# Optimization experiments

Hardware: AMD Instinct MI355X
Metric: run time of the kernel (lower is better)

The kernel has to match this reference:

```python
import jax, jax.numpy as jnp
import numpy as np

R, N, B, S = 20, 4096, 16, 256          # relations, total nodes, graphs, nodes per graph
DIN, HID, H = 512, 128, 4               # in_dim, hidden_dim, num_heads
D = HID * H                              # flattened node-feature width (=512)
E = 16384                                # edges per relation
NEG_SLOPE = 0.2


def _gat(h, src, dst, W, al, ar, b):
    # DGL GATConv, eval mode (dropout off), identity residual (in == H*out), allow_zero_in_degree
    z = (h @ W).reshape(N, H, HID)                        # [N,H,Dh]
    el = (z * al).sum(-1)                                 # [N,H]
    er = (z * ar).sum(-1)                                 # [N,H]
    e = jax.nn.leaky_relu(el[src] + er[dst], NEG_SLOPE)   # [E,H]
    m = jax.ops.segment_max(e, dst, num_segments=N)       # per-dst max (edge softmax)
    ex = jnp.exp(e - m[dst])
    den = jax.ops.segment_sum(ex, dst, num_segments=N)
    alpha = ex / den[dst]                                 # [E,H]
    agg = jax.ops.segment_sum(alpha[..., None] * z[src], dst, num_segments=N)
    return agg + h.reshape(N, H, HID) + b, alpha


def _rgat_conv(h, src, dst, W, al, ar, b):
    # HeteroGraphConv with aggregate='mean' over R relations; scan keeps memory flat
    def body(acc, xs):
        s, d, Wr, alr, arr, br = xs
        out, alpha = _gat(h, s, d, Wr, alr, arr, br)
        return acc + out, alpha.mean(-1)                  # attention meaned over heads -> [E]
    acc, attn = jax.lax.scan(body, jnp.zeros((N, H, HID), h.dtype), (src, dst, W, al, ar, b))
    return acc / R, attn                                  # [N,H,Dh], [R,E]


def setup_inputs() -> dict:
    key = jax.random.key(0)
    ks = jax.random.split(key, 24)
    f32 = jnp.float32
    p = lambda k, shape: jax.random.normal(k, shape, f32) * 0.05
    z = lambda shape: jnp.zeros(shape, f32)
    return {
        'feat': jax.random.normal(ks[0], (N, DIN), f32),
        'hyp_emb': jax.random.normal(ks[1], (B, D), f32),
        'edge_src': jax.random.randint(ks[2], (R, E), 0, N),
        'edge_dst': jax.random.randint(ks[3], (R, E), 0, N),
        'W1': p(ks[4], (R, DIN, H * HID)), 'al1': p(ks[5], (R, H, HID)), 'ar1': p(ks[6], (R, H, HID)), 'b1': z((R, H, HID)),
        'W2': p(ks[7], (R, D, H * HID)), 'al2': p(ks[8], (R, H, HID)), 'ar2': p(ks[9], (R, H, HID)), 'b2': z((R, H, HID)),
        'Wq': p(ks[10], (D, D)), 'bq': z(D), 'Wk': p(ks[11], (D, D)), 'bk': z(D),
        'Wv': p(ks[12], (D, D)), 'bv': z(D), 'Wo': p(ks[13], (D, D)), 'bo': z(D),
        'Wn1': p(ks[14], (2 * D, HID)), 'bn1': z(HID), 'Wn2': p(ks[15], (HID, 2)), 'bn2': z(2),
    }


def reference(feat, hyp_emb, edge_src, edge_dst,
              W1, al1, ar1, b1, W2, al2, ar2, b2,
              Wq, bq, Wk, bk, Wv, bv, Wo, bo, Wn1, bn1, Wn2, bn2):
    # --- RGAT (rgat_generation) layer 1 + attention weights ---
    h1, attn = _rgat_conv(feat, edge_src, edge_dst, W1, al1, ar1, b1)
    h1 = jax.nn.elu(h1.reshape(N, D))
    # --- layer 2 ---
    h2, _ = _rgat_conv(h1, edge_src, edge_dst, W2, al2, ar2, b2)
    feats = h2.reshape(N, D)
    # --- node importance: scatter-add edge attention onto dst nodes, summed over etypes ---
    imp = jax.ops.segment_sum(attn.reshape(-1), edge_dst.reshape(-1), num_segments=N)
    feats_p = feats.reshape(B, S, D)                      # uniform graphs: split+pad == reshape
    weighted = feats_p * imp.reshape(B, S)[..., None]
    # --- MultiheadAttention(embed=D, heads=4): query = hyp_emb broadcast to all S positions ---
    Hm, Dm = 4, D // 4
    q = (hyp_emb @ Wq + bq).reshape(B, Hm, 1, Dm)         # identical query at every position
    k = (feats_p @ Wk + bk).reshape(B, S, Hm, Dm).transpose(0, 2, 1, 3)
    v = (feats_p @ Wv + bv).reshape(B, S, Hm, Dm).transpose(0, 2, 1, 3)
    scores = jnp.einsum('bhqd,bhkd->bhqk', q, k) / jnp.sqrt(jnp.float32(Dm))
    a = jax.nn.softmax(scores, axis=-1)                   # [B,Hm,1,S]
    ctx = jnp.einsum('bhqk,bhkd->bhqd', a, v).reshape(B, 1, D)
    attn_out = jnp.broadcast_to(ctx @ Wo + bo, (B, S, D))
    # --- node classifier on concat(weighted feats, attention output) ---
    combined = jnp.concatenate([weighted, attn_out], axis=-1).reshape(N, 2 * D)
    node_logits = jax.nn.relu(combined @ Wn1 + bn1) @ Wn2 + bn2
    return node_logits, attn
```

## Files before the change

### kernel.cpp

```cpp
#include <hip/hip_runtime.h>
#include <hip/hip_bf16.h>
#include <math.h>

#define NREL 20
#define NN   4096
#define NE   16384
#define DF   512
#define NHD  4
#define DHH  128
#define NB   16
#define NS   256

typedef __attribute__((ext_vector_type(8))) __bf16 bf16x8;
typedef __attribute__((ext_vector_type(4))) float f32x4;
typedef __attribute__((ext_vector_type(2))) float f32x2;

struct f8 { unsigned char b; };

__device__ inline float bf2f(unsigned short u) {
    union { float f; unsigned int i; } c; c.i = ((unsigned int)u) << 16; return c.f;
}
__device__ inline unsigned short f2bu(float f) {
    union { __hip_bfloat16 b; unsigned short u; } c; c.b = __float2bfloat16(f); return c.u;
}
__device__ inline void storeOut(float* p, float v) { *p = v; }
__device__ inline void storeOut(__hip_bfloat16* p, float v) { *p = __float2bfloat16(v); }

__device__ inline void load_lds16(const __hip_bfloat16* g, __hip_bfloat16* l) {
    __builtin_amdgcn_global_load_lds(
        (const __attribute__((address_space(1))) unsigned int*)(const void*)g,
        (__attribute__((address_space(3))) unsigned int*)(void*)l, 16, 0, 0);
}

__device__ inline int kswz(int f, int row) { return f ^ (((row) & 7) << 3); }

__global__ __launch_bounds__(256) void prep_kernel(
    const float* __restrict__ feat, unsigned short* __restrict__ featbf,
    const float* __restrict__ b1, const float* __restrict__ b2,
    const float* __restrict__ bk, const float* __restrict__ bv,
    float* __restrict__ bsum1, float* __restrict__ bsum2,
    float* __restrict__ bkv, int* __restrict__ cnt, float* __restrict__ imp)
{
    int blk = blockIdx.x, t = threadIdx.x;
    if (blk < 1024) {
        int idx = blk * 256 + t;
        int row = idx >> 6;
        int f = (idx & 63) * 8;
        int fs = kswz(f, row);
        const float4* ip = (const float4*)&feat[(size_t)row * DF + f];
        float4 v0 = ip[0], v1 = ip[1];
        union { unsigned short u[8]; uint4 q; } o;
        o.u[0] = f2bu(v0.x); o.u[1] = f2bu(v0.y); o.u[2] = f2bu(v0.z); o.u[3] = f2bu(v0.w);
        o.u[4] = f2bu(v1.x); o.u[5] = f2bu(v1.y); o.u[6] = f2bu(v1.z); o.u[7] = f2bu(v1.w);
        *(uint4*)(featbf + (size_t)row * DF + fs) = o.q;
    } else if (blk == 1024) {
        #pragma unroll
        for (int rep = 0; rep < 2; ++rep) {
            int f = t + rep * 256;
            float s1 = 0.f, s2 = 0.f;
            #pragma unroll
            for (int r = 0; r < NREL; ++r) { s1 += b1[r * DF + f]; s2 += b2[r * DF + f]; }
            bsum1[f] = s1; bsum2[f] = s2;
        }
        for (int i = t; i < NN; i += 256) imp[i] = 0.f;
    } else if (blk == 1025) {
        #pragma unroll
        for (int j = 0; j < 4; ++j) {
            int f = t + j * 256;
            bkv[f] = (f < DF) ? bk[f] : bv[f - DF];
        }
    } else {
        int idx = (blk - 1026) * 256 + t;
        cnt[idx] = 0;
    }
}

__global__ void count_kernel(const int* __restrict__ dst, int* __restrict__ cnt) {
    int idx = blockIdx.x * 256 + threadIdx.x;
    int r = idx / NE;
    atomicAdd(&cnt[r * NN + dst[idx]], 1);
}

__global__ void scan_kernel(const int* __restrict__ cnt, int* __restrict__ rowptr,
                            int* __restrict__ woff, int* __restrict__ rowptr2,
                            int* __restrict__ croff) {
    int r = blockIdx.x;
    int t = threadIdx.x;
    __shared__ int sums[1024];
    int v[4]; int local = 0;
    if (r < NREL) {
        #pragma unroll
        for (int j = 0; j < 4; ++j) { v[j] = cnt[r * NN + t * 4 + j]; local += v[j]; }
    } else {
        #pragma unroll
        for (int j = 0; j < 4; ++j) {
            int s = 0;
            for (int rel = 0; rel < NREL; ++rel) {
                croff[rel * NN + t * 4 + j] = s;
                s += cnt[rel * NN + t * 4 + j];
            }
            v[j] = s; local += s;
        }
    }
    sums[t] = local;
    __syncthreads();
    for (int off = 1; off < 1024; off <<= 1) {
        int x = (t >= off) ? sums[t - off] : 0;
        __syncthreads();
        sums[t] += x;
        __syncthreads();
    }
    int run = (t == 0) ? 0 : sums[t - 1];
    if (r < NREL) {
        #pragma unroll
        for (int j = 0; j < 4; ++j) {
            rowptr[r * (NN + 1) + t * 4 + j] = run;
            woff[r * NN + t * 4 + j] = run;
            run += v[j];
        }
        if (t == 1023) rowptr[r * (NN + 1) + NN] = run;
    } else {
        #pragma unroll
        for (int j = 0; j < 4; ++j) { rowptr2[t * 4 + j] = run; run += v[j]; }
        if (t == 1023) rowptr2[NN] = run;
    }
}

__global__ void fill_kernel(const int* __restrict__ dst, const int* __restrict__ src,
                            int* __restrict__ woff, int* __restrict__ srcCSR,
                            int* __restrict__ eidCSR) {
    int idx = blockIdx.x * 256 + threadIdx.x;
    int r = idx / NE; int e = idx % NE;
    int pos = atomicAdd(&woff[r * NN + dst[idx]], 1);
    srcCSR[r * NE + pos] = src[idx];
    eidCSR[r * NE + pos] = e;
}

__global__ __launch_bounds__(256) void transw_kernel(
    const float* __restrict__ W, __hip_bfloat16* __restrict__ Wt, int K, int N)
{
    int r = blockIdx.z;
    __shared__ float t[32][33];
    int k0 = blockIdx.x * 32, n0 = blockIdx.y * 32;
    int tx = threadIdx.x % 32, ty = threadIdx.x / 32;
    #pragma unroll
    for (int kk = ty; kk < 32; kk += 8)
        t[kk][tx] = W[((size_t)r * K + k0 + kk) * N + n0 + tx];
    __syncthreads();
    #pragma unroll
    for (int nn = ty; nn < 32; nn += 8) {
        int row = n0 + nn;
        Wt[((size_t)r * N + row) * K + kswz(k0 + tx, row)] = __float2bfloat16(t[tx][nn]);
    }
}

__global__ __launch_bounds__(256) void transw2_kernel(
    const float* __restrict__ W1, const float* __restrict__ W2,
    __hip_bfloat16* __restrict__ Wt1, __hip_bfloat16* __restrict__ Wt2)
{
    int z = blockIdx.z;
    const float* W = (z < NREL) ? W1 : W2;
    __hip_bfloat16* Wt = (z < NREL) ? Wt1 : Wt2;
    int r = (z < NREL) ? z : z - NREL;
    __shared__ float t[32][33];
    int k0 = blockIdx.x * 32, n0 = blockIdx.y * 32;
    int tx = threadIdx.x % 32, ty = threadIdx.x / 32;
    #pragma unroll
    for (int kk = ty; kk < 32; kk += 8)
        t[kk][tx] = W[((size_t)r * DF + k0 + kk) * DF + n0 + tx];
    __syncthreads();
    #pragma unroll
    for (int nn = ty; nn < 32; nn += 8) {
        int row = n0 + nn;
        Wt[((size_t)r * DF + row) * DF + kswz(k0 + tx, row)] = __float2bfloat16(t[tx][nn]);
    }
}

__global__ __launch_bounds__(256) void transw_kv_kernel(
    const float* __restrict__ Wk, const float* __restrict__ Wv,
    __hip_bfloat16* __restrict__ Wt)
{
    int z = blockIdx.z;
    const float* W = z ? Wv : Wk;
    __shared__ float t[32][33];
    int k0 = blockIdx.x * 32, n0 = blockIdx.y * 32;
    int tx = threadIdx.x % 32, ty = threadIdx.x / 32;
    #pragma unroll
    for (int kk = ty; kk < 32; kk += 8)
        t[kk][tx] = W[(size_t)(k0 + kk) * DF + n0 + tx];
    __syncthreads();
    #pragma unroll
    for (int nn = ty; nn < 32; nn += 8) {
        int row = n0 + nn;
        Wt[((size_t)z * DF + row) * DF + kswz(k0 + tx, row)] = __float2bfloat16(t[tx][nn]);
    }
}

template <typename OutT, bool RELU, bool FUSE, bool SPLITK = false>
__global__ __launch_bounds__(256) void mfma_gemm(
    const __hip_bfloat16* __restrict__ A,
    const __hip_bfloat16* __restrict__ BtAll,
    const float* __restrict__ bias, int biasStride,
    OutT* __restrict__ Call, int M, int N, int K, int lda,
    const float* __restrict__ al, const float* __restrict__ ar,
    float* __restrict__ el, float* __restrict__ er)
{
    int r = blockIdx.z;
    const __hip_bfloat16* Bt;
    int koff;
    if (SPLITK) { Bt = BtAll;                         koff = r * K; }
    else        { Bt = BtAll + (size_t)r * N * lda;   koff = 0; }
    OutT* C = Call + (size_t)r * M * N;
    const int rowBase = blockIdx.y * 128;
    const int colBase = blockIdx.x * 128;
    __shared__ __hip_bfloat16 As[128 * 64];
    __shared__ __hip_bfloat16 Bs[128 * 64];
    const int tid = threadIdx.x;
    const int w = tid >> 6, l = tid & 63;
    const int wr = w >> 1, wc = w & 1;
    const int m15 = l & 15, q = l >> 4;
    const int sRow = tid >> 3;
    const int sChk = tid & 7;
    const __hip_bfloat16* Ag = A + (size_t)(rowBase + sRow) * lda + koff + sChk * 8;
    const __hip_bfloat16* Bg = Bt + (size_t)(colBase + sRow) * lda + koff + sChk * 8;
    __hip_bfloat16* Asl = As + tid * 8;
    __hip_bfloat16* Bsl = Bs + tid * 8;
    const int swr = m15 & 7;

    f32x4 acc[4][4];
    #pragma unroll
    for (int i = 0; i < 4; ++i)
        #pragma unroll
        for (int j = 0; j < 4; ++j) acc[i][j] = (f32x4){0.f, 0.f, 0.f, 0.f};

    for (int k0 = 0; k0 < K; k0 += 64) {
        #pragma unroll
        for (int c = 0; c < 4; ++c) {
            load_lds16(Ag + (size_t)c * 32 * lda + k0, Asl + c * 2048);
            load_lds16(Bg + (size_t)c * 32 * lda + k0, Bsl + c * 2048);
        }
        __syncthreads();
        #pragma unroll
        for (int g = 0; g < 2; ++g) {
            bf16x8 a[4], b[4];
            #pragma unroll
            for (int i = 0; i < 4; ++i)
                a[i] = *(const bf16x8*)&As[(wr * 64 + i * 16 + m15) * 64 + ((g * 4 + q) ^ swr) * 8];
            #pragma unroll
            for (int j = 0; j < 4; ++j)
                b[j] = *(const bf16x8*)&Bs[(wc * 64 + j * 16 + m15) * 64 + ((g * 4 + q) ^ swr) * 8];
            #pragma unroll
            for (int i = 0; i < 4; ++i)
                #pragma unroll
                for (int j = 0; j < 4; ++j)
                    acc[i][j] = __builtin_amdgcn_mfma_f32_16x16x32_bf16(a[i], b[j], acc[i][j], 0, 0, 0);
        }
        __syncthreads();
    }

    if constexpr (sizeof(OutT) == 1) {
        unsigned char* cbuf = (unsigned char*)As;
        #pragma unroll
        for (int i = 0; i < 4; ++i)
            #pragma unroll
            for (int j = 0; j < 4; ++j) {
                int colL = wc * 64 + j * 16 + m15;
                #pragma unroll
                for (int reg = 0; reg < 4; ++reg) {
                    int rowL = wr * 64 + i * 16 + q * 4 + reg;
                    unsigned int pk = __builtin_amdgcn_cvt_pk_fp8_f32(
                        acc[i][j][reg], acc[i][j][reg], 0, false);
                    cbuf[rowL * 128 + colL] = (unsigned char)(pk & 0xFF);
                }
            }
        __syncthreads();
        int rowL = tid >> 1, colL = (tid & 1) * 64;
        const uint4* src = (const uint4*)&cbuf[rowL * 128 + colL];
        uint4* dst = (uint4*)((unsigned char*)C + (size_t)(rowBase + rowL) * N
                              + colBase + colL);
        #pragma unroll
        for (int x = 0; x < 4; ++x) dst[x] = src[x];
    } else {
        #pragma unroll
        for (int i = 0; i < 4; ++i) {
            #pragma unroll
            for (int j = 0; j < 4; ++j) {
                int col = colBase + wc * 64 + j * 16 + m15;
                float bv = bias ? bias[r * biasStride + col] : 0.f;
                #pragma unroll
                for (int reg = 0; reg < 4; ++reg) {
                    int row = rowBase + wr * 64 + i * 16 + q * 4 + reg;
                    float v = acc[i][j][reg] + bv;
                    if (RELU) v = fmaxf(v, 0.f);
                    storeOut(&C[(size_t)row * N + col], v);
                }
            }
        }
    }

    if (FUSE) {
        float alv[4], arv[4];
        #pragma unroll
        for (int j = 0; j < 4; ++j) {
            int col = colBase + wc * 64 + j * 16 + m15;
            alv[j] = al[r * DF + col];
            arv[j] = ar[r * DF + col];
        }
        float pe[4][4], pr[4][4];
        #pragma unroll
        for (int i = 0; i < 4; ++i)
            #pragma unroll
            for (int reg = 0; reg < 4; ++reg) {
                float se = 0.f, sr = 0.f;
                #pragma unroll
                for (int j = 0; j < 4; ++j) {
                    se += acc[i][j][reg] * alv[j];
                    sr += acc[i][j][reg] * arv[j];
                }
                pe[i][reg] = se; pr[i][reg] = sr;
            }
        #pragma unroll
        for (int off = 1; off < 16; off <<= 1)
            #pragma unroll
            for (int i = 0; i < 4; ++i)
                #pragma unroll
                for (int reg = 0; reg < 4; ++reg) {
                    pe[i][reg] += __shfl_xor(pe[i][reg], off);
                    pr[i][reg] += __shfl_xor(pr[i][reg], off);
                }
        float* eP = (float*)Bs;
        float* rP = eP + 256;
        if (m15 == 0) {
            #pragma unroll
            for (int i = 0; i < 4; ++i)
                #pragma unroll
                for (int reg = 0; reg < 4; ++reg) {
                    int rowL = wr * 64 + i * 16 + q * 4 + reg;
                    eP[rowL * 2 + wc] = pe[i][reg];
                    rP[rowL * 2 + wc] = pr[i][reg];
                }
        }
        __syncthreads();
        if (tid < 128) {
            int head = colBase >> 7;
            size_t idx = ((size_t)r * NN + rowBase + tid) * NHD + head;
            el[idx] = eP[tid * 2] + eP[tid * 2 + 1];
            er[idx] = rP[tid * 2] + rP[tid * 2 + 1];
        }
    }
}

template <typename OutT>
__global__ __launch_bounds__(256) void gemm_kernel(
    const float* __restrict__ A, const float* __restrict__ Bm,
    const float* __restrict__ bias, OutT* __restrict__ C,
    int M, int K, int Nn)
{
    int r = blockIdx.z;
    const float* B = Bm + (size_t)r * K * Nn;
    OutT* Cr = C + (size_t)r * M * Nn;
    int rowBase = blockIdx.y * 64;
    int colBase = blockIdx.x * 64;
    __shared__ float As[64][17];
    __shared__ float Bs[16][64];
    int tid = threadIdx.x;
    int tx = tid % 16, ty = tid / 16;
    float acc[4][4] = {};
    int aRow = tid / 4, aK4 = (tid % 4) * 4;
    int bK = tid / 16, bN4 = (tid % 16) * 4;
    for (int k0 = 0; k0 < K; k0 += 16) {
        int gRow = rowBase + aRow;
        float4 av = make_float4(0.f, 0.f, 0.f, 0.f);
        if (gRow < M) av = *(const float4*)(A + (size_t)gRow * K + k0 + aK4);
        As[aRow][aK4 + 0] = av.x; As[aRow][aK4 + 1] = av.y;
        As[aRow][aK4 + 2] = av.z; As[aRow][aK4 + 3] = av.w;
        float4 bv = *(const float4*)(B + (size_t)(k0 + bK) * Nn + colBase + bN4);
        *(float4*)&Bs[bK][bN4] = bv;
        __syncthreads();
        #pragma unroll
        for (int k = 0; k < 16; ++k) {
            float a[4], b[4];
            #pragma unroll
            for (int i = 0; i < 4; ++i) a[i] = As[ty * 4 + i][k];
            #pragma unroll
            for (int j = 0; j < 4; ++j) b[j] = Bs[k][tx * 4 + j];
            #pragma unroll
            for (int i = 0; i < 4; ++i)
                #pragma unroll
                for (int j = 0; j < 4; ++j) acc[i][j] += a[i] * b[j];
        }
        __syncthreads();
    }
    #pragma unroll
    for (int i = 0; i < 4; ++i) {
        int gRow = rowBase + ty * 4 + i;
        if (gRow >= M) continue;
        #pragma unroll
        for (int j = 0; j < 4; ++j) {
            int gCol = colBase + tx * 4 + j;
            float v = acc[i][j];
            if (bias) v += bias[gCol];
            storeOut(&Cr[(size_t)gRow * Nn + gCol], v);
        }
    }
}

__global__ __launch_bounds__(256) void alpha_kernel(
    const float* __restrict__ el, const float* __restrict__ er,
    const int* __restrict__ rowptr, const int* __restrict__ rowptr2,
    const int* __restrict__ croff, const int* __restrict__ srcCSR,
    const int* __restrict__ eidCSR,
    float* __restrict__ alphaPk, int* __restrict__ srcPk,
    float* __restrict__ attn, float* __restrict__ imp)
{
    int t = blockIdx.x * 256 + threadIdx.x;
    int r = t / NN, n = t % NN;
    int start = rowptr[r * (NN + 1) + n];
    int d = rowptr[r * (NN + 1) + n + 1] - start;
    if (d == 0) return;
    int pbase = rowptr2[n] + croff[r * NN + n];
    float4 er4 = *(const float4*)&er[((size_t)r * NN + n) * NHD];
    float4 den = make_float4(0.f, 0.f, 0.f, 0.f);
    for (int j = 0; j < d; ++j) {
        int s = srcCSR[r * NE + start + j];
        float4 el4 = *(const float4*)&el[((size_t)r * NN + s) * NHD];
        float v0 = el4.x + er4.x; v0 = v0 > 0.f ? v0 : 0.2f * v0;
        float v1 = el4.y + er4.y; v1 = v1 > 0.f ? v1 : 0.2f * v1;
        float v2 = el4.z + er4.z; v2 = v2 > 0.f ? v2 : 0.2f * v2;
        float v3 = el4.w + er4.w; v3 = v3 > 0.f ? v3 : 0.2f * v3;
        float4 e4 = make_float4(__expf(v0), __expf(v1), __expf(v2), __expf(v3));
        den.x += e4.x; den.y += e4.y; den.z += e4.z; den.w += e4.w;
        *(float4*)&alphaPk[(size_t)(pbase + j) * 4] = e4;
        srcPk[pbase + j] = r * NN + s;
    }
    float4 inv = make_float4(1.f / den.x, 1.f / den.y, 1.f / den.z, 1.f / den.w);
    float impLoc = 0.f;
    for (int j = 0; j < d; ++j) {
        float4 a4 = *(const float4*)&alphaPk[(size_t)(pbase + j) * 4];
        a4.x *= inv.x; a4.y *= inv.y; a4.z *= inv.z; a4.w *= inv.w;
        *(float4*)&alphaPk[(size_t)(pbase + j) * 4] = a4;
        if (attn) {
            float a = 0.25f * (a4.x + a4.y + a4.z + a4.w);
            attn[r * NE + eidCSR[r * NE + start + j]] = a;
            impLoc += a;
        }
    }
    if (attn) atomicAdd(&imp[n], impLoc);
}

__global__ __launch_bounds__(256) void aggc_kernel(
    const unsigned char* __restrict__ Z,
    const int* __restrict__ rowptr2, const int* __restrict__ srcPk,
    const float* __restrict__ alphaPk, const float* __restrict__ bsum,
    const float* __restrict__ hin, float* __restrict__ hout,
    __hip_bfloat16* __restrict__ hout_bf, int applyElu)
{
    int n = blockIdx.x;
    int w = threadIdx.x >> 6, lane = threadIdx.x & 63;
    int h = lane >> 4;
    int base = rowptr2[n];
    int deg = rowptr2[n + 1] - base;
    float acc[8] = {};
    if (deg > 0) {
        int i = w * 4;
        int zz[4]; float aa[4];
        #pragma unroll
        for (int j = 0; j < 4; ++j) {
            int idx = i + j; int cidx = idx < deg ? idx : deg - 1;
            zz[j] = srcPk[base + cidx];
            aa[j] = (idx < deg) ? alphaPk[(size_t)(base + cidx) * 4 + h] : 0.f;
        }
        while (i < deg) {
            int cz[4]; float ca[4];
            #pragma unroll
            for (int j = 0; j < 4; ++j) { cz[j] = zz[j]; ca[j] = aa[j]; }
            int ni = i + 16;
            #pragma unroll
            for (int j = 0; j < 4; ++j) {
                int idx = ni + j; int cidx = idx < deg ? idx : deg - 1;
                zz[j] = srcPk[base + cidx];
                aa[j] = (idx < deg) ? alphaPk[(size_t)(base + cidx) * 4 + h] : 0.f;
            }
            uint2 raw[4];
            #pragma unroll
            for (int j = 0; j < 4; ++j)
                raw[j] = *(const uint2*)&Z[(size_t)cz[j] * DF + lane * 8];
            #pragma unroll
            for (int j = 0; j < 4; ++j) {
                f32x2 f01 = __builtin_amdgcn_cvt_pk_f32_fp8((int)raw[j].x, false);
                f32x2 f23 = __builtin_amdgcn_cvt_pk_f32_fp8((int)raw[j].x, true);
                f32x2 f45 = __builtin_amdgcn_cvt_pk_f32_fp8((int)raw[j].y, false);
                f32x2 f67 = __builtin_amdgcn_cvt_pk_f32_fp8((int)raw[j].y, true);
                acc[0] += ca[j] * f01.x; acc[1] += ca[j] * f01.y;
                acc[2] += ca[j] * f23.x; acc[3] += ca[j] * f23.y;
                acc[4] += ca[j] * f45.x; acc[5] += ca[j] * f45.y;
                acc[6] += ca[j] * f67.x; acc[7] += ca[j] * f67.y;
            }
            i = ni;
        }
    }
    __shared__ float red[4][DF];
    #pragma unroll
    for (int j = 0; j < 8; ++j) red[w][lane * 8 + j] = acc[j];
    __syncthreads();
    const float invR = 1.0f / NREL;
    const int sw = (n & 7) << 3;
    int f = threadIdx.x;
    #pragma unroll
    for (int rep = 0; rep < 2; ++rep, f += 256) {
        float v = red[0][f] + red[1][f] + red[2][f] + red[3][f];
        v = (v + bsum[f]) * invR + hin[(size_t)n * DF + f];
        if (applyElu) v = v > 0.f ? v : expm1f(v);
        hout[(size_t)n * DF + f] = v;
        hout_bf[(size_t)n * DF + (f ^ sw)] = __float2bfloat16(v);
    }
}

__global__ __launch_bounds__(256) void mha_scores(
    const float* __restrict__ q, const float* __restrict__ k,
    float* __restrict__ scores)
{
    int b = blockIdx.x;
    int w = threadIdx.x >> 6, lane = threadIdx.x & 63;
    int s = blockIdx.y * 4 + w;
    const float4* qp = (const float4*)&q[(size_t)b * DF + lane * 8];
    const float4* kp = (const float4*)&k[((size_t)(b * NS + s)) * DF + lane * 8];
    float4 q0 = qp[0], q1 = qp[1];
    float4 k0 = kp[0], k1 = kp[1];
    float p = q0.x * k0.x + q0.y * k0.y + q0.z * k0.z + q0.w * k0.w
            + q1.x * k1.x + q1.y * k1.y + q1.z * k1.z + q1.w * k1.w;
    #pragma unroll
    for (int off = 1; off < 16; off <<= 1) p += __shfl_xor(p, off);
    if ((lane & 15) == 0) {
        int h = lane >> 4;
        scores[((size_t)(b * NHD + h)) * NS + s] = p * 0.08838834764831845f;
    }
}

__global__ __launch_bounds__(256) void mha_soft(float* __restrict__ scores) {
    int b = blockIdx.x;
    int h = threadIdx.x >> 6, lane = threadIdx.x & 63;
    float* sp = &scores[((size_t)(b * NHD + h)) * NS];
    float v[4];
    float mx = -INFINITY;
    #pragma unroll
    for (int i = 0; i < 4; ++i) { v[i] = sp[lane + 64 * i]; mx = fmaxf(mx, v[i]); }
    #pragma unroll
    for (int off = 32; off; off >>= 1) mx = fmaxf(mx, __shfl_xor(mx, off));
    float sum = 0.f;
    #pragma unroll
    for (int i = 0; i < 4; ++i) { v[i] = __expf(v[i] - mx); sum += v[i]; }
    #pragma unroll
    for (int off = 32; off; off >>= 1) sum += __shfl_xor(sum, off);
    float inv = 1.0f / sum;
    #pragma unroll
    for (int i = 0; i < 4; ++i) sp[lane + 64 * i] = v[i] * inv;
}

__global__ __launch_bounds__(256) void mha_ctx(
    const float* __restrict__ scores, const float* __restrict__ v,
    float* __restrict__ ctx)
{
    int b = blockIdx.x, h = blockIdx.y;
    int t = threadIdx.x;
    int d = t & 127, half = t >> 7;
    __shared__ float a_s[NS];
    a_s[t] = scores[((size_t)(b * NHD + h)) * NS + t];
    __syncthreads();
    float acc = 0.f;
    const float* vp = &v[((size_t)(b * NS + half * 128)) * DF + h * DHH + d];
    #pragma unroll 4
    for (int i = 0; i < 128; ++i)
        acc += a_s[half * 128 + i] * vp[(size_t)i * DF];
    __shared__ float red[256];
    red[t] = acc;
    __syncthreads();
    if (t < 128) ctx[(size_t)b * DF + h * DHH + t] = red[t] + red[t + 128];
}

__global__ __launch_bounds__(256) void combined_kernel(
    const float* __restrict__ feats, const float* __restrict__ imp,
    const float* __restrict__ abuf, __hip_bfloat16* __restrict__ comb)
{
    int n = blockIdx.x;
    int t = threadIdx.x;
    int b = n >> 8;
    float im = imp[n];
    const int sw = (n & 7) << 3;
    #pragma unroll
    for (int rep = 0; rep < 4; ++rep) {
        int f = t + rep * 256;
        float v = (f < DF) ? feats[(size_t)n * DF + f] * im
                           : abuf[(size_t)b * DF + (f - DF)];
        comb[(size_t)n * (2 * DF) + (f ^ sw)] = __float2bfloat16(v);
    }
}

__global__ __launch_bounds__(256) void cls2_kernel(
    const float* __restrict__ hidden4, const float* __restrict__ bn1,
    const float* __restrict__ Wn2, const float* __restrict__ bn2,
    float* __restrict__ out)
{
    __shared__ float w2[256];
    __shared__ float b1s[128];
    int t = threadIdx.x;
    w2[t] = Wn2[t];
    if (t < 128) b1s[t] = bn1[t];
    __syncthreads();
    int n = blockIdx.x * 256 + t;
    const float* hp = &hidden4[(size_t)n * 128];
    const size_t ps = (size_t)NN * 128;
    float p0 = bn2[0], p1 = bn2[1];
    #pragma unroll 4
    for (int kk = 0; kk < 128; ++kk) {
        float hv = hp[kk] + hp[ps + kk] + hp[2 * ps + kk] + hp[3 * ps + kk] + b1s[kk];
        hv = fmaxf(hv, 0.f);
        p0 += hv * w2[kk * 2 + 0];
        p1 += hv * w2[kk * 2 + 1];
    }
    out[n * 2 + 0] = p0;
    out[n * 2 + 1] = p1;
}

extern "C" void kernel_launch(void* const* d_in, const int* in_sizes, int n_in,
                              void* d_out, int out_size, void* d_ws, size_t ws_size,
                              hipStream_t stream) {
    const float* feat = (const float*)d_in[0];
    const float* hyp  = (const float*)d_in[1];
    const int*   esrc = (const int*)d_in[2];
    const int*   edst = (const int*)d_in[3];
    const float* W1   = (const float*)d_in[4];
    const float* al1  = (const float*)d_in[5];
    const float* ar1  = (const float*)d_in[6];
    const float* b1   = (const float*)d_in[7];
    const float* W2   = (const float*)d_in[8];
    const float* al2  = (const float*)d_in[9];
    const float* ar2  = (const float*)d_in[10];
    const float* b2   = (const float*)d_in[11];
    const float* Wq = (const float*)d_in[12]; const float* bq = (const float*)d_in[13];
    const float* Wk = (const float*)d_in[14]; const float* bk = (const float*)d_in[15];
    const float* Wv = (const float*)d_in[16]; const float* bv = (const float*)d_in[17];
    const float* Wo = (const float*)d_in[18]; const float* bo = (const float*)d_in[19];
    const float* Wn1 = (const float*)d_in[20]; const float* bn1 = (const float*)d_in[21];
    const float* Wn2 = (const float*)d_in[22]; const float* bn2 = (const float*)d_in[23];

    char* ws = (char*)d_ws;
    size_t off = 0;
    auto alloc = [&](size_t bytes) -> void* {
        void* p = ws + off;
        off += (bytes + 255) & ~(size_t)255;
        return p;
    };
    unsigned char* Z = (unsigned char*)alloc((size_t)NREL * NN * DF);
    float* el     = (float*)alloc((size_t)NREL * NN * NHD * 4);
    float* er     = (float*)alloc((size_t)NREL * NN * NHD * 4);
    int* rowptr   = (int*)alloc((size_t)NREL * (NN + 1) * 4);
    int* rowptr2  = (int*)alloc((size_t)(NN + 1) * 4);
    int* woff     = (int*)alloc((size_t)NREL * NN * 4);
    int* srcCSR   = (int*)alloc((size_t)NREL * NE * 4);
    int* eidCSR   = (int*)alloc((size_t)NREL * NE * 4);
    int* cnt      = (int*)alloc((size_t)NREL * NN * 4);
    int* croff    = (int*)alloc((size_t)NREL * NN * 4);
    int* srcPk    = (int*)alloc((size_t)NREL * NE * 4);
    float* alphaPk= (float*)alloc((size_t)NREL * NE * NHD * 4);
    float* bsum1  = (float*)alloc((size_t)DF * 4);
    float* bsum2  = (float*)alloc((size_t)DF * 4);
    float* bkv    = (float*)alloc((size_t)2 * DF * 4);
    float* h1     = (float*)alloc((size_t)NN * DF * 4);
    float* feats  = (float*)alloc((size_t)NN * DF * 4);
    float* imp    = (float*)alloc((size_t)NN * 4);
    float* kvbuf  = (float*)alloc((size_t)2 * NN * DF * 4);
    float* qbuf   = (float*)alloc((size_t)NB * DF * 4);
    float* ctxb   = (float*)alloc((size_t)NB * DF * 4);
    float* abuf   = (float*)alloc((size_t)NB * DF * 4);
    float* scoresb= (float*)alloc((size_t)NB * NHD * NS * 4);
    float* hidden4= (float*)alloc((size_t)4 * NN * 128 * 4);
    __hip_bfloat16* featbf  = (__hip_bfloat16*)alloc((size_t)NN * DF * 2);
    __hip_bfloat16* h1bf    = (__hip_bfloat16*)alloc((size_t)NN * DF * 2);
    __hip_bfloat16* featsbf = (__hip_bfloat16*)alloc((size_t)NN * DF * 2);
    __hip_bfloat16* combbf  = (__hip_bfloat16*)alloc((size_t)NN * 2 * DF * 2);
    __hip_bfloat16* Wt1 = (__hip_bfloat16*)alloc((size_t)NREL * DF * DF * 2);
    __hip_bfloat16* Wt2 = (__hip_bfloat16*)alloc((size_t)NREL * DF * DF * 2);
    __hip_bfloat16* WtKV = (__hip_bfloat16*)alloc((size_t)2 * DF * DF * 2);
    __hip_bfloat16* Wn1t = (__hip_bfloat16*)alloc((size_t)(2 * DF) * 128 * 2);
    if (off > ws_size) return;

    float* logits = (float*)d_out;
    float* attn   = (float*)d_out + (size_t)NN * 2;
    float* kbuf = kvbuf;
    float* vbuf = kvbuf + (size_t)NN * DF;

    prep_kernel<<<1026 + NREL * NN / 256, 256, 0, stream>>>(
        feat, (unsigned short*)featbf, b1, b2, bk, bv, bsum1, bsum2, bkv, cnt, imp);

    count_kernel<<<NREL * NE / 256, 256, 0, stream>>>(edst, cnt);
    scan_kernel<<<NREL + 1, 1024, 0, stream>>>(cnt, rowptr, woff, rowptr2, croff);
    fill_kernel<<<NREL * NE / 256, 256, 0, stream>>>(edst, esrc, woff, srcCSR, eidCSR);

    transw2_kernel<<<dim3(DF / 32, DF / 32, 2 * NREL), 256, 0, stream>>>(W1, W2, Wt1, Wt2);
    transw_kv_kernel<<<dim3(DF / 32, DF / 32, 2), 256, 0, stream>>>(Wk, Wv, WtKV);
    transw_kernel<<<dim3(2 * DF / 32, 128 / 32, 1), 256, 0, stream>>>(Wn1, Wn1t, 2 * DF, 128);

    mfma_gemm<f8, false, true><<<dim3(DF / 128, NN / 128, NREL), 256, 0, stream>>>(
        featbf, Wt1, nullptr, 0, (f8*)Z, NN, DF, DF, DF, al1, ar1, el, er);
    alpha_kernel<<<NREL * NN / 256, 256, 0, stream>>>(
        el, er, rowptr, rowptr2, croff, srcCSR, eidCSR, alphaPk, srcPk, attn, imp);
    aggc_kernel<<<NN, 256, 0, stream>>>(Z, rowptr2, srcPk, alphaPk, bsum1,
                                        feat, h1, h1bf, 1);

    mfma_gemm<f8, false, true><<<dim3(DF / 128, NN / 128, NREL), 256, 0, stream>>>(
        h1bf, Wt2, nullptr, 0, (f8*)Z, NN, DF, DF, DF, al2, ar2, el, er);
    alpha_kernel<<<NREL * NN / 256, 256, 0, stream>>>(
        el, er, rowptr, rowptr2, croff, srcCSR, eidCSR, alphaPk, srcPk, nullptr, nullptr);
    aggc_kernel<<<NN, 256, 0, stream>>>(Z, rowptr2, srcPk, alphaPk, bsum2,
                                        h1, feats, featsbf, 0);

    mfma_gemm<float, false, false><<<dim3(DF / 128, NN / 128, 2), 256, 0, stream>>>(
        featsbf, WtKV, bkv, DF, kvbuf, NN, DF, DF, DF, nullptr, nullptr, nullptr, nullptr);
    gemm_kernel<float><<<dim3(DF / 64, 1, 1), 256, 0, stream>>>(
        hyp, Wq, bq, qbuf, NB, DF, DF);
    mha_scores<<<dim3(NB, NS / 4), 256, 0, stream>>>(qbuf, kbuf, scoresb);
    mha_soft<<<NB, 256, 0, stream>>>(scoresb);
    mha_ctx<<<dim3(NB, NHD), 256, 0, stream>>>(scoresb, vbuf, ctxb);
    gemm_kernel<float><<<dim3(DF / 64, 1, 1), 256, 0, stream>>>(
        ctxb, Wo, bo, abuf, NB, DF, DF);

    combined_kernel<<<NN, 256, 0, stream>>>(feats, imp, abuf, combbf);
    mfma_gemm<float, false, false, true><<<dim3(1, NN / 128, 4), 256, 0, stream>>>(
        combbf, Wn1t, nullptr, 0, hidden4, NN, 128, 256, 2 * DF,
        nullptr, nullptr, nullptr, nullptr);
    cls2_kernel<<<NN / 256, 256, 0, stream>>>(hidden4, bn1, Wn2, bn2, logits);
}
```

Measured before the change: 577.4 us.

## Replace per-relation GAT projection GEMM with 256x256 double-buffered MFMA kernel

Adds a specialized zgemm8 kernel with 256x256 tiles, 512 threads, double-buffered LDS staging and interleaved MFMA phases. It emits FP8 Z through an LDS-staged coalesced store and fuses the el/er attention-logit reductions into the epilogue. The change also merges the K/V weight transpose into the W1/W2 transpose launch and folds the MHA softmax into mha_ctx, removing two launches. The larger tile improves operand reuse, but it cuts the grid to 2x16x20 blocks and raises register and LDS pressure, which may hurt occupancy.

```diff
diff --git a/kernel.cpp b/kernel.cpp
--- a/kernel.cpp
+++ b/kernel.cpp
@@ -156,43 +156,219 @@
 
 __global__ __launch_bounds__(256) void transw2_kernel(
     const float* __restrict__ W1, const float* __restrict__ W2,
-    __hip_bfloat16* __restrict__ Wt1, __hip_bfloat16* __restrict__ Wt2)
+    const float* __restrict__ Wk, const float* __restrict__ Wv,
+    __hip_bfloat16* __restrict__ Wt1, __hip_bfloat16* __restrict__ Wt2,
+    __hip_bfloat16* __restrict__ WtKV)
 {
     int z = blockIdx.z;
-    const float* W = (z < NREL) ? W1 : W2;
-    __hip_bfloat16* Wt = (z < NREL) ? Wt1 : Wt2;
-    int r = (z < NREL) ? z : z - NREL;
+    const float* Wsrc; __hip_bfloat16* Wdst;
+    if (z < NREL)           { Wsrc = W1 + (size_t)z * DF * DF;          Wdst = Wt1 + (size_t)z * DF * DF; }
+    else if (z < 2 * NREL)  { Wsrc = W2 + (size_t)(z - NREL) * DF * DF; Wdst = Wt2 + (size_t)(z - NREL) * DF * DF; }
+    else if (z == 2 * NREL) { Wsrc = Wk;                                Wdst = WtKV; }
+    else                    { Wsrc = Wv;                                Wdst = WtKV + (size_t)DF * DF; }
     __shared__ float t[32][33];
     int k0 = blockIdx.x * 32, n0 = blockIdx.y * 32;
     int tx = threadIdx.x % 32, ty = threadIdx.x / 32;
     #pragma unroll
     for (int kk = ty; kk < 32; kk += 8)
-        t[kk][tx] = W[((size_t)r * DF + k0 + kk) * DF + n0 + tx];
+        t[kk][tx] = Wsrc[(size_t)(k0 + kk) * DF + n0 + tx];
     __syncthreads();
     #pragma unroll
     for (int nn = ty; nn < 32; nn += 8) {
         int row = n0 + nn;
-        Wt[((size_t)r * DF + row) * DF + kswz(k0 + tx, row)] = __float2bfloat16(t[tx][nn]);
-    }
-}
-
-__global__ __launch_bounds__(256) void transw_kv_kernel(
-    const float* __restrict__ Wk, const float* __restrict__ Wv,
-    __hip_bfloat16* __restrict__ Wt)
-{
-    int z = blockIdx.z;
-    const float* W = z ? Wv : Wk;
-    __shared__ float t[32][33];
-    int k0 = blockIdx.x * 32, n0 = blockIdx.y * 32;
-    int tx = threadIdx.x % 32, ty = threadIdx.x / 32;
-    #pragma unroll
-    for (int kk = ty; kk < 32; kk += 8)
-        t[kk][tx] = W[(size_t)(k0 + kk) * DF + n0 + tx];
-    __syncthreads();
-    #pragma unroll
-    for (int nn = ty; nn < 32; nn += 8) {
-        int row = n0 + nn;
-        Wt[((size_t)z * DF + row) * DF + kswz(k0 + tx, row)] = __float2bfloat16(t[tx][nn]);
+        Wdst[(size_t)row * DF + kswz(k0 + tx, row)] = __float2bfloat16(t[tx][nn]);
+    }
+}
+
+__global__ __launch_bounds__(512) void zgemm8(
+    const __hip_bfloat16* __restrict__ A,
+    const __hip_bfloat16* __restrict__ BtAll,
+    unsigned char* __restrict__ Zall,
+    const float* __restrict__ al, const float* __restrict__ ar,
+    float* __restrict__ el, float* __restrict__ er)
+{
+    const int r = blockIdx.z;
+    const __hip_bfloat16* Bt = BtAll + (size_t)r * DF * DF;
+    unsigned char* Z = Zall + (size_t)r * NN * DF;
+    const int rowBase = blockIdx.y * 256;
+    const int colBase = blockIdx.x * 256;
+    __shared__ __hip_bfloat16 As[2][256][64];
+    __shared__ __hip_bfloat16 Bs[2][256][64];
+    const int tid = threadIdx.x;
+    const int w = tid >> 6, l = tid & 63;
+    const int wr = w >> 2, wc = w & 3;
+    const int m15 = l & 15, q = l >> 4;
+    const int swr = m15 & 7;
+
+    const __hip_bfloat16* Ag = A + (size_t)(rowBase + (tid >> 3)) * DF + (tid & 7) * 8;
+    const __hip_bfloat16* Bg = Bt + (size_t)(colBase + (tid >> 3)) * DF + (tid & 7) * 8;
+    __hip_bfloat16* AsT = &As[0][0][0] + tid * 8;
+    __hip_bfloat16* BsT = &Bs[0][0][0] + tid * 8;
+
+#define STAGE_A(buf, half, kt) do { \
+        const __hip_bfloat16* s_ = Ag + (size_t)((half) * 128) * DF + (kt) * 64; \
+        __hip_bfloat16* d_ = AsT + (buf) * 16384 + (half) * 8192; \
+        load_lds16(s_, d_); \
+        load_lds16(s_ + (size_t)64 * DF, d_ + 4096); } while (0)
+#define STAGE_B(buf, half, kt) do { \
+        const __hip_bfloat16* s_ = Bg + (size_t)((half) * 128) * DF + (kt) * 64; \
+        __hip_bfloat16* d_ = BsT + (buf) * 16384 + (half) * 8192; \
+        load_lds16(s_, d_); \
+        load_lds16(s_ + (size_t)64 * DF, d_ + 4096); } while (0)
+
+    f32x4 acc[8][4];
+    #pragma unroll
+    for (int i = 0; i < 8; ++i)
+        #pragma unroll
+        for (int j = 0; j < 4; ++j) acc[i][j] = (f32x4){0.f, 0.f, 0.f, 0.f};
+
+    const int NT = DF / 64;
+    STAGE_A(0, 0, 0); STAGE_A(0, 1, 0); STAGE_B(0, 0, 0); STAGE_B(0, 1, 0);
+    STAGE_A(1, 0, 1); STAGE_A(1, 1, 1);
+    asm volatile("s_waitcnt vmcnt(4)" ::: "memory");
+    __builtin_amdgcn_s_barrier();
+    __builtin_amdgcn_sched_barrier(0);
+
+    bf16x8 a0[8], a1[8], b0[4], b1[4];
+    for (int kt = 0; kt < NT; ++kt) {
+        const int buf = kt & 1, obuf = buf ^ 1;
+        #pragma unroll
+        for (int i = 0; i < 8; ++i)
+            a0[i] = *(const bf16x8*)&As[buf][wr * 128 + i * 16 + m15][(q ^ swr) * 8];
+        #pragma unroll
+        for (int j = 0; j < 4; ++j)
+            b0[j] = *(const bf16x8*)&Bs[buf][wc * 64 + j * 16 + m15][(q ^ swr) * 8];
+        if (kt + 1 < NT) STAGE_B(obuf, 0, kt + 1);
+        __builtin_amdgcn_s_barrier();
+        asm volatile("s_waitcnt lgkmcnt(0)" ::: "memory");
+        __builtin_amdgcn_sched_barrier(0);
+        __builtin_amdgcn_s_setprio(1);
+        #pragma unroll
+        for (int i = 0; i < 4; ++i)
+            #pragma unroll
+            for (int j = 0; j < 4; ++j)
+                acc[i][j] = __builtin_amdgcn_mfma_f32_16x16x32_bf16(a0[i], b0[j], acc[i][j], 0, 0, 0);
+        __builtin_amdgcn_s_setprio(0);
+        __builtin_amdgcn_s_barrier();
+        #pragma unroll
+        for (int i = 0; i < 8; ++i)
+            a1[i] = *(const bf16x8*)&As[buf][wr * 128 + i * 16 + m15][((4 + q) ^ swr) * 8];
+        if (kt + 1 < NT) STAGE_B(obuf, 1, kt + 1);
+        __builtin_amdgcn_s_barrier();
+        asm volatile("s_waitcnt lgkmcnt(0)" ::: "memory");
+        __builtin_amdgcn_sched_barrier(0);
+        __builtin_amdgcn_s_setprio(1);
+        #pragma unroll
+        for (int i = 4; i < 8; ++i)
+            #pragma unroll
+            for (int j = 0; j < 4; ++j)
+                acc[i][j] = __builtin_amdgcn_mfma_f32_16x16x32_bf16(a0[i], b0[j], acc[i][j], 0, 0, 0);
+        __builtin_amdgcn_s_setprio(0);
+        __builtin_amdgcn_s_barrier();
+        #pragma unroll
+        for (int j = 0; j < 4; ++j)
+            b1[j] = *(const bf16x8*)&Bs[buf][wc * 64 + j * 16 + m15][((4 + q) ^ swr) * 8];
+        if (kt + 2 < NT) STAGE_A(buf, 0, kt + 2);
+        __builtin_amdgcn_s_barrier();
+        asm volatile("s_waitcnt lgkmcnt(0)" ::: "memory");
+        __builtin_amdgcn_sched_barrier(0);
+        __builtin_amdgcn_s_setprio(1);
+        #pragma unroll
+        for (int i = 0; i < 4; ++i)
+            #pragma unroll
+            for (int j = 0; j < 4; ++j)
+                acc[i][j] = __builtin_amdgcn_mfma_f32_16x16x32_bf16(a1[i], b1[j], acc[i][j], 0, 0, 0);
+        __builtin_amdgcn_s_setprio(0);
+        __builtin_amdgcn_s_barrier();
+        if (kt + 2 < NT) STAGE_A(buf, 1, kt + 2);
+        __builtin_amdgcn_s_barrier();
+        __builtin_amdgcn_s_setprio(1);
+        #pragma unroll
+        for (int i = 4; i < 8; ++i)
+            #pragma unroll
+            for (int j = 0; j < 4; ++j)
+                acc[i][j] = __builtin_amdgcn_mfma_f32_16x16x32_bf16(a1[i], b1[j], acc[i][j], 0, 0, 0);
+        __builtin_amdgcn_s_setprio(0);
+        if (kt + 2 < NT) { asm volatile("s_waitcnt vmcnt(4)" ::: "memory"); }
+        else             { asm volatile("s_waitcnt vmcnt(0)" ::: "memory"); }
+        __builtin_amdgcn_s_barrier();
+        __builtin_amdgcn_sched_barrier(0);
+    }
+#undef STAGE_A
+#undef STAGE_B
+
+    unsigned char* cbuf = (unsigned char*)&As[0][0][0];
+    #pragma unroll
+    for (int i = 0; i < 8; ++i)
+        #pragma unroll
+        for (int j = 0; j < 4; ++j) {
+            int colL = wc * 64 + j * 16 + m15;
+            #pragma unroll
+            for (int reg = 0; reg < 4; ++reg) {
+                int rowL = wr * 128 + i * 16 + q * 4 + reg;
+                unsigned int pk = __builtin_amdgcn_cvt_pk_fp8_f32(
+                    acc[i][j][reg], acc[i][j][reg], 0, false);
+                cbuf[rowL * 256 + colL] = (unsigned char)(pk & 0xFF);
+            }
+        }
+    __syncthreads();
+    {
+        int rowL = tid >> 1, colL = (tid & 1) * 128;
+        const uint4* src = (const uint4*)&cbuf[rowL * 256 + colL];
+        uint4* dst = (uint4*)(Z + (size_t)(rowBase + rowL) * DF + colBase + colL);
+        #pragma unroll
+        for (int x = 0; x < 8; ++x) dst[x] = src[x];
+    }
+
+    float alv[4], arv[4];
+    #pragma unroll
+    for (int j = 0; j < 4; ++j) {
+        int col = colBase + wc * 64 + j * 16 + m15;
+        alv[j] = al[r * DF + col];
+        arv[j] = ar[r * DF + col];
+    }
+    float pe[8][4], pr[8][4];
+    #pragma unroll
+    for (int i = 0; i < 8; ++i)
+        #pragma unroll
+        for (int reg = 0; reg < 4; ++reg) {
+            float se = 0.f, sr = 0.f;
+            #pragma unroll
+            for (int j = 0; j < 4; ++j) {
+                se += acc[i][j][reg] * alv[j];
+                sr += acc[i][j][reg] * arv[j];
+            }
+            pe[i][reg] = se; pr[i][reg] = sr;
+        }
+    #pragma unroll
+    for (int off = 1; off < 16; off <<= 1)
+        #pragma unroll
+        for (int i = 0; i < 8; ++i)
+            #pragma unroll
+            for (int reg = 0; reg < 4; ++reg) {
+                pe[i][reg] += __shfl_xor(pe[i][reg], off);
+                pr[i][reg] += __shfl_xor(pr[i][reg], off);
+            }
+    float* eP = (float*)&Bs[0][0][0];
+    float* rP = eP + 1024;
+    if (m15 == 0) {
+        int hh = wc >> 1, strip = wc & 1;
+        #pragma unroll
+        for (int i = 0; i < 8; ++i)
+            #pragma unroll
+            for (int reg = 0; reg < 4; ++reg) {
+                int rowL = wr * 128 + i * 16 + q * 4 + reg;
+                eP[(hh * 256 + rowL) * 2 + strip] = pe[i][reg];
+                rP[(hh * 256 + rowL) * 2 + strip] = pr[i][reg];
+            }
+    }
+    __syncthreads();
+    {
+        int rowL = tid & 255, hh = tid >> 8;
+        int head = (colBase >> 7) + hh;
+        size_t idx = ((size_t)r * NN + rowBase + rowL) * NHD + head;
+        el[idx] = eP[(hh * 256 + rowL) * 2] + eP[(hh * 256 + rowL) * 2 + 1];
+        er[idx] = rP[(hh * 256 + rowL) * 2] + rP[(hh * 256 + rowL) * 2 + 1];
     }
 }
 
@@ -537,36 +713,32 @@
     }
 }
 
-__global__ __launch_bounds__(256) void mha_soft(float* __restrict__ scores) {
-    int b = blockIdx.x;
-    int h = threadIdx.x >> 6, lane = threadIdx.x & 63;
-    float* sp = &scores[((size_t)(b * NHD + h)) * NS];
-    float v[4];
-    float mx = -INFINITY;
-    #pragma unroll
-    for (int i = 0; i < 4; ++i) { v[i] = sp[lane + 64 * i]; mx = fmaxf(mx, v[i]); }
-    #pragma unroll
-    for (int off = 32; off; off >>= 1) mx = fmaxf(mx, __shfl_xor(mx, off));
-    float sum = 0.f;
-    #pragma unroll
-    for (int i = 0; i < 4; ++i) { v[i] = __expf(v[i] - mx); sum += v[i]; }
-    #pragma unroll
-    for (int off = 32; off; off >>= 1) sum += __shfl_xor(sum, off);
-    float inv = 1.0f / sum;
-    #pragma unroll
-    for (int i = 0; i < 4; ++i) sp[lane + 64 * i] = v[i] * inv;
-}
-
 __global__ __launch_bounds__(256) void mha_ctx(
     const float* __restrict__ scores, const float* __restrict__ v,
     float* __restrict__ ctx)
 {
     int b = blockIdx.x, h = blockIdx.y;
     int t = threadIdx.x;
+    int lane = t & 63, w = t >> 6;
+    __shared__ float a_s[NS];
+    __shared__ float wred[8];
+    float sv = scores[((size_t)(b * NHD + h)) * NS + t];
+    float mx = sv;
+    #pragma unroll
+    for (int off = 1; off < 64; off <<= 1) mx = fmaxf(mx, __shfl_xor(mx, off));
+    if (lane == 0) wred[w] = mx;
+    __syncthreads();
+    mx = fmaxf(fmaxf(wred[0], wred[1]), fmaxf(wred[2], wred[3]));
+    float e = __expf(sv - mx);
+    float sum = e;
+    #pragma unroll
+    for (int off = 1; off < 64; off <<= 1) sum += __shfl_xor(sum, off);
+    if (lane == 0) wred[4 + w] = sum;
+    __syncthreads();
+    sum = wred[4] + wred[5] + wred[6] + wred[7];
+    a_s[t] = e * (1.0f / sum);
+    __syncthreads();
     int d = t & 127, half = t >> 7;
-    __shared__ float a_s[NS];
-    a_s[t] = scores[((size_t)(b * NHD + h)) * NS + t];
-    __syncthreads();
     float acc = 0.f;
     const float* vp = &v[((size_t)(b * NS + half * 128)) * DF + h * DHH + d];
     #pragma unroll 4
@@ -697,19 +869,19 @@
     scan_kernel<<<NREL + 1, 1024, 0, stream>>>(cnt, rowptr, woff, rowptr2, croff);
     fill_kernel<<<NREL * NE / 256, 256, 0, stream>>>(edst, esrc, woff, srcCSR, eidCSR);
 
-    transw2_kernel<<<dim3(DF / 32, DF / 32, 2 * NREL), 256, 0, stream>>>(W1, W2, Wt1, Wt2);
-    transw_kv_kernel<<<dim3(DF / 32, DF / 32, 2), 256, 0, stream>>>(Wk, Wv, WtKV);
+    transw2_kernel<<<dim3(DF / 32, DF / 32, 2 * NREL + 2), 256, 0, stream>>>(
+        W1, W2, Wk, Wv, Wt1, Wt2, WtKV);
     transw_kernel<<<dim3(2 * DF / 32, 128 / 32, 1), 256, 0, stream>>>(Wn1, Wn1t, 2 * DF, 128);
 
-    mfma_gemm<f8, false, true><<<dim3(DF / 128, NN / 128, NREL), 256, 0, stream>>>(
-        featbf, Wt1, nullptr, 0, (f8*)Z, NN, DF, DF, DF, al1, ar1, el, er);
+    zgemm8<<<dim3(DF / 256, NN / 256, NREL), 512, 0, stream>>>(
+        featbf, Wt1, Z, al1, ar1, el, er);
     alpha_kernel<<<NREL * NN / 256, 256, 0, stream>>>(
         el, er, rowptr, rowptr2, croff, srcCSR, eidCSR, alphaPk, srcPk, attn, imp);
     aggc_kernel<<<NN, 256, 0, stream>>>(Z, rowptr2, srcPk, alphaPk, bsum1,
                                         feat, h1, h1bf, 1);
 
-    mfma_gemm<f8, false, true><<<dim3(DF / 128, NN / 128, NREL), 256, 0, stream>>>(
-        h1bf, Wt2, nullptr, 0, (f8*)Z, NN, DF, DF, DF, al2, ar2, el, er);
+    zgemm8<<<dim3(DF / 256, NN / 256, NREL), 512, 0, stream>>>(
+        h1bf, Wt2, Z, al2, ar2, el, er);
     alpha_kernel<<<NREL * NN / 256, 256, 0, stream>>>(
         el, er, rowptr, rowptr2, croff, srcCSR, eidCSR, alphaPk, srcPk, nullptr, nullptr);
     aggc_kernel<<<NN, 256, 0, stream>>>(Z, rowptr2, srcPk, alphaPk, bsum2,
@@ -720,7 +892,6 @@
     gemm_kernel<float><<<dim3(DF / 64, 1, 1), 256, 0, stream>>>(
         hyp, Wq, bq, qbuf, NB, DF, DF);
     mha_scores<<<dim3(NB, NS / 4), 256, 0, stream>>>(qbuf, kbuf, scoresb);
-    mha_soft<<<NB, 256, 0, stream>>>(scoresb);
     mha_ctx<<<dim3(NB, NHD), 256, 0, stream>>>(scoresb, vbuf, ctxb);
     gemm_kernel<float><<<dim3(DF / 64, 1, 1), 256, 0, stream>>>(
         ctxb, Wo, bo, abuf, NB, DF, DF);
```

Result: no change. 584.7 us (+1.3%).
